# Kernel optimization log

Measured on AMD Instinct MI355X. Metric: run time of the kernel, lower is better.

## Reference

```python
import jax, jax.numpy as jnp
import numpy as np

GRID_RES = (8, 8, 4)      # probe grid -> 256 probes
GRID_MIN = 0.0
GRID_MAX = 1.0
RES = 128                  # cubemap face resolution (max_res)
N_QUERY = 524288


def _cube_face_uv(d):
    """Map unit directions [N,3] -> (face id [N], u [N], v [N]) with the standard
    OpenGL/nvdiffrast cubemap convention (boundary_mode='cube')."""
    x, y, z = d[:, 0], d[:, 1], d[:, 2]
    ax, ay, az = jnp.abs(x), jnp.abs(y), jnp.abs(z)
    is_x = (ax >= ay) & (ax >= az)
    is_y = (~is_x) & (ay >= az)
    face = jnp.where(is_x, jnp.where(x >= 0, 0, 1),
           jnp.where(is_y, jnp.where(y >= 0, 2, 3),
                           jnp.where(z >= 0, 4, 5))).astype(jnp.int32)
    ma = jnp.maximum(jnp.where(is_x, ax, jnp.where(is_y, ay, az)), 1e-9)
    sc = jnp.where(is_x, jnp.where(x >= 0, -z, z),
         jnp.where(is_y, x, jnp.where(z >= 0, x, -x)))
    tc = jnp.where(is_x, -y, jnp.where(is_y, jnp.where(y >= 0, z, -z), -y))
    u = 0.5 * (sc / ma + 1.0)
    v = 0.5 * (tc / ma + 1.0)
    return face, u, v


def _trilinear_corners(xyz):
    """Faithful port of MultiEnvLight._compute_trilinear_corners.
    xyz: [N,3] -> (corner probe indices [N,8] int32, normalized weights [N,8])."""
    res_f = jnp.array(GRID_RES, dtype=jnp.float32)
    res_i = jnp.array(GRID_RES, dtype=jnp.int32)
    span = jnp.maximum(GRID_MAX - GRID_MIN, 1e-6)
    coord = (xyz - GRID_MIN) / span * (res_f - 1.0)
    coord = jnp.clip(coord, 0.0, res_f - 1.0)
    i0 = jnp.floor(coord).astype(jnp.int32)
    i1 = jnp.minimum(i0 + 1, res_i - 1)
    t = coord - i0.astype(jnp.float32)
    # 8 corner offsets (ox, oy, oz)
    offs = jnp.array([[ox, oy, oz] for ox in (0, 1) for oy in (0, 1) for oz in (0, 1)],
                     dtype=jnp.int32)                                  # [8,3]
    idx = jnp.where(offs[None] == 1, i1[:, None, :], i0[:, None, :])   # [N,8,3]
    w = jnp.prod(jnp.where(offs[None] == 1, t[:, None, :], 1.0 - t[:, None, :]), axis=-1)  # [N,8]
    stride_x = GRID_RES[1] * GRID_RES[2]
    stride_y = GRID_RES[2]
    flat = idx[..., 0] * stride_x + idx[..., 1] * stride_y + idx[..., 2]  # [N,8]
    w = w / jnp.maximum(jnp.sum(w, axis=1, keepdims=True), 1e-8)
    return flat, w


def setup_inputs() -> dict:
    key = jax.random.key(0)
    k1, k2, k3 = jax.random.split(key, 3)
    xyz = jax.random.uniform(k1, (N_QUERY, 3), dtype=jnp.float32)
    l = jax.random.normal(k2, (N_QUERY, 3), dtype=jnp.float32)
    n_probes = GRID_RES[0] * GRID_RES[1] * GRID_RES[2]
    base = jax.random.normal(k3, (n_probes, 6, RES, RES, 3), dtype=jnp.float32)
    return {"xyz": xyz, "l": l, "base": base}


def reference(xyz, l, base):
    """MultiEnvLight forward, 'pure_env' mode: trilinear k-NN probe selection over
    the grid + bilinear cube-texture sampling of each selected probe's cubemap,
    weighted blend, then sigmoid()*10 (EnvLight output transform)."""
    R = RES
    d = l / jnp.maximum(jnp.linalg.norm(l, axis=-1, keepdims=True), 1e-9)
    face, u, v = _cube_face_uv(d)
    # bilinear texel footprint (clamp-to-edge within the face)
    fx = u * R - 0.5
    fy = v * R - 0.5
    x0f = jnp.floor(fx)
    y0f = jnp.floor(fy)
    tx = fx - x0f
    ty = fy - y0f
    x0 = jnp.clip(x0f.astype(jnp.int32), 0, R - 1)
    x1 = jnp.clip(x0f.astype(jnp.int32) + 1, 0, R - 1)
    y0 = jnp.clip(y0f.astype(jnp.int32), 0, R - 1)
    y1 = jnp.clip(y0f.astype(jnp.int32) + 1, 0, R - 1)

    pidx, pw = _trilinear_corners(xyz)                       # [N,8], [N,8]
    probe_off = pidx * (6 * R * R) + face[:, None] * (R * R)  # [N,8]
    tap = jnp.stack([y0 * R + x0, y0 * R + x1, y1 * R + x0, y1 * R + x1], axis=-1)  # [N,4]
    taps = probe_off[:, :, None] + tap[:, None, :]            # [N,8,4]
    tapw = jnp.stack([(1.0 - ty) * (1.0 - tx), (1.0 - ty) * tx,
                      ty * (1.0 - tx), ty * tx], axis=-1)     # [N,4]

    vals = base.reshape(-1, 3)[taps]                          # [N,8,4,3] gather
    bil = jnp.einsum('nt,nptc->npc', tapw, vals)              # bilinear per probe
    light = jnp.einsum('np,npc->nc', pw, bil)                 # blend 8 corner probes
    return jax.nn.sigmoid(light) * 10.0
```

## Files before the change

kernel.cpp:

```cpp
#include <hip/hip_runtime.h>
#include <math.h>

#define RES 128

__global__ __launch_bounds__(256) void mel_kernel(
    const float* __restrict__ xyz, const float* __restrict__ l,
    const float* __restrict__ base, float* __restrict__ out, int n)
{
    int i = blockIdx.x * blockDim.x + threadIdx.x;
    if (i >= n) return;

    float lx = l[3*i+0], ly = l[3*i+1], lz = l[3*i+2];
    float nrm = sqrtf(lx*lx + ly*ly + lz*lz);
    float inv = 1.0f / fmaxf(nrm, 1e-9f);
    float dx = lx*inv, dy = ly*inv, dz = lz*inv;

    float ax = fabsf(dx), ay = fabsf(dy), az = fabsf(dz);
    bool is_x = (ax >= ay) && (ax >= az);
    bool is_y = (!is_x) && (ay >= az);

    int face;
    float ma, sc, tc;
    if (is_x) {
        face = (dx >= 0.0f) ? 0 : 1;
        ma = ax;
        sc = (dx >= 0.0f) ? -dz : dz;
        tc = -dy;
    } else if (is_y) {
        face = (dy >= 0.0f) ? 2 : 3;
        ma = ay;
        sc = dx;
        tc = (dy >= 0.0f) ? dz : -dz;
    } else {
        face = (dz >= 0.0f) ? 4 : 5;
        ma = az;
        sc = (dz >= 0.0f) ? dx : -dx;
        tc = -dy;
    }
    ma = fmaxf(ma, 1e-9f);
    float u = 0.5f * (sc / ma + 1.0f);
    float v = 0.5f * (tc / ma + 1.0f);

    float fx = u * (float)RES - 0.5f;
    float fy = v * (float)RES - 0.5f;
    float x0f = floorf(fx), y0f = floorf(fy);
    float tx = fx - x0f, ty = fy - y0f;
    int x0 = min(max((int)x0f,     0), RES-1);
    int x1 = min(max((int)x0f + 1, 0), RES-1);
    int y0 = min(max((int)y0f,     0), RES-1);
    int y1 = min(max((int)y0f + 1, 0), RES-1);

    float px = xyz[3*i+0], py = xyz[3*i+1], pz = xyz[3*i+2];
    float cx = fminf(fmaxf(px * 7.0f, 0.0f), 7.0f);
    float cy = fminf(fmaxf(py * 7.0f, 0.0f), 7.0f);
    float cz = fminf(fmaxf(pz * 3.0f, 0.0f), 3.0f);
    int ix0 = (int)floorf(cx), iy0 = (int)floorf(cy), iz0 = (int)floorf(cz);
    int ix1 = min(ix0 + 1, 7), iy1 = min(iy0 + 1, 7), iz1 = min(iz0 + 1, 3);
    float tgx = cx - (float)ix0, tgy = cy - (float)iy0, tgz = cz - (float)iz0;

    float wx[2] = {1.0f - tgx, tgx};
    float wy[2] = {1.0f - tgy, tgy};
    float wz[2] = {1.0f - tgz, tgz};
    int   gx[2] = {ix0, ix1}, gy[2] = {iy0, iy1}, gz[2] = {iz0, iz1};

    float pw[8];
    int   pidx[8];
    float wsum = 0.0f;
    #pragma unroll
    for (int ox = 0; ox < 2; ++ox)
      #pragma unroll
      for (int oy = 0; oy < 2; ++oy)
        #pragma unroll
        for (int oz = 0; oz < 2; ++oz) {
            int p = ox*4 + oy*2 + oz;
            float w = wx[ox] * wy[oy] * wz[oz];
            pw[p]   = w;
            wsum   += w;
            pidx[p] = gx[ox]*32 + gy[oy]*4 + gz[oz];
        }
    float winv = 1.0f / fmaxf(wsum, 1e-8f);

    int t00 = y0*RES + x0;
    int t01 = y0*RES + x1;
    int t10 = y1*RES + x0;
    int t11 = y1*RES + x1;
    float bw[4];
    bw[0] = (1.0f - ty) * (1.0f - tx);
    bw[1] = (1.0f - ty) * tx;
    bw[2] = ty * (1.0f - tx);
    bw[3] = ty * tx;

    int face_off = face * (RES * RES);
    int toff[4] = {t00, t01, t10, t11};

    float vals[8][4][3];
    #pragma unroll
    for (int p = 0; p < 8; ++p) {
        const float* bp = base + (size_t)(pidx[p] * (6 * RES * RES) + face_off) * 3;
        #pragma unroll
        for (int t = 0; t < 4; ++t) {
            const float* a = bp + toff[t] * 3;
            vals[p][t][0] = a[0];
            vals[p][t][1] = a[1];
            vals[p][t][2] = a[2];
        }
    }

    __builtin_amdgcn_sched_barrier(0);

    float acc0 = 0.0f, acc1 = 0.0f, acc2 = 0.0f;
    #pragma unroll
    for (int p = 0; p < 8; ++p) {
        float w = pw[p];
        #pragma unroll
        for (int t = 0; t < 4; ++t) {
            float wt = w * bw[t];
            acc0 += wt * vals[p][t][0];
            acc1 += wt * vals[p][t][1];
            acc2 += wt * vals[p][t][2];
        }
    }
    acc0 *= winv; acc1 *= winv; acc2 *= winv;

    float s0 = 10.0f / (1.0f + __expf(-acc0));
    float s1 = 10.0f / (1.0f + __expf(-acc1));
    float s2 = 10.0f / (1.0f + __expf(-acc2));

    out[3*i+0] = s0;
    out[3*i+1] = s1;
    out[3*i+2] = s2;
}

extern "C" void kernel_launch(void* const* d_in, const int* in_sizes, int n_in,
                              void* d_out, int out_size, void* d_ws, size_t ws_size,
                              hipStream_t stream) {
    const float* xyz  = (const float*)d_in[0];
    const float* l    = (const float*)d_in[1];
    const float* base = (const float*)d_in[2];
    float* out = (float*)d_out;
    int n = in_sizes[0] / 3;
    int blocks = (n + 255) / 256;
    mel_kernel<<<blocks, 256, 0, stream>>>(xyz, l, base, out, n);
}
```

Baseline: 500.4 us.

## Split each query across four lanes, one per xy probe pair, shuffle-reduce

Each query is now handled by four threads, each gathering the two probes (z corners) for one xy corner, instead of one thread gathering all eight probes. Partial sums and weight sums are combined with xor shuffles, and lane 0 applies the normalization and sigmoid. This cuts per-thread register pressure and serial gather latency to raise occupancy and memory-level parallelism. In exchange, the cubemap direction and grid math is repeated in all four lanes, and three of every four lanes sit idle during the store.

```diff
diff --git a/kernel.cpp b/kernel.cpp
--- a/kernel.cpp
+++ b/kernel.cpp
@@ -7,10 +7,12 @@
     const float* __restrict__ xyz, const float* __restrict__ l,
     const float* __restrict__ base, float* __restrict__ out, int n)
 {
-    int i = blockIdx.x * blockDim.x + threadIdx.x;
-    if (i >= n) return;
+    int tid = blockIdx.x * blockDim.x + threadIdx.x;
+    int q   = tid >> 2;
+    int sub = tid & 3;
+    if (q >= n) return;
 
-    float lx = l[3*i+0], ly = l[3*i+1], lz = l[3*i+2];
+    float lx = l[3*q+0], ly = l[3*q+1], lz = l[3*q+2];
     float nrm = sqrtf(lx*lx + ly*ly + lz*lz);
     float inv = 1.0f / fmaxf(nrm, 1e-9f);
     float dx = lx*inv, dy = ly*inv, dz = lz*inv;
@@ -50,7 +52,7 @@
     int y0 = min(max((int)y0f,     0), RES-1);
     int y1 = min(max((int)y0f + 1, 0), RES-1);
 
-    float px = xyz[3*i+0], py = xyz[3*i+1], pz = xyz[3*i+2];
+    float px = xyz[3*q+0], py = xyz[3*q+1], pz = xyz[3*q+2];
     float cx = fminf(fmaxf(px * 7.0f, 0.0f), 7.0f);
     float cy = fminf(fmaxf(py * 7.0f, 0.0f), 7.0f);
     float cz = fminf(fmaxf(pz * 3.0f, 0.0f), 3.0f);
@@ -58,32 +60,19 @@
     int ix1 = min(ix0 + 1, 7), iy1 = min(iy0 + 1, 7), iz1 = min(iz0 + 1, 3);
     float tgx = cx - (float)ix0, tgy = cy - (float)iy0, tgz = cz - (float)iz0;
 
-    float wx[2] = {1.0f - tgx, tgx};
-    float wy[2] = {1.0f - tgy, tgy};
-    float wz[2] = {1.0f - tgz, tgz};
-    int   gx[2] = {ix0, ix1}, gy[2] = {iy0, iy1}, gz[2] = {iz0, iz1};
+    int   ox  = sub >> 1, oy = sub & 1;
+    float wxf = ox ? tgx : (1.0f - tgx);
+    float wyf = oy ? tgy : (1.0f - tgy);
+    int   gxi = ox ? ix1 : ix0;
+    int   gyi = oy ? iy1 : iy0;
+    float wxy = wxf * wyf;
+    float pw0 = wxy * (1.0f - tgz);
+    float pw1 = wxy * tgz;
+    int   gb  = gxi*32 + gyi*4;
+    int   p0  = gb + iz0;
+    int   p1  = gb + iz1;
 
-    float pw[8];
-    int   pidx[8];
-    float wsum = 0.0f;
-    #pragma unroll
-    for (int ox = 0; ox < 2; ++ox)
-      #pragma unroll
-      for (int oy = 0; oy < 2; ++oy)
-        #pragma unroll
-        for (int oz = 0; oz < 2; ++oz) {
-            int p = ox*4 + oy*2 + oz;
-            float w = wx[ox] * wy[oy] * wz[oz];
-            pw[p]   = w;
-            wsum   += w;
-            pidx[p] = gx[ox]*32 + gy[oy]*4 + gz[oz];
-        }
-    float winv = 1.0f / fmaxf(wsum, 1e-8f);
-
-    int t00 = y0*RES + x0;
-    int t01 = y0*RES + x1;
-    int t10 = y1*RES + x0;
-    int t11 = y1*RES + x1;
+    int toff[4] = { y0*RES + x0, y0*RES + x1, y1*RES + x0, y1*RES + x1 };
     float bw[4];
     bw[0] = (1.0f - ty) * (1.0f - tx);
     bw[1] = (1.0f - ty) * tx;
@@ -91,44 +80,46 @@
     bw[3] = ty * tx;
 
     int face_off = face * (RES * RES);
-    int toff[4] = {t00, t01, t10, t11};
+    const float* bp0 = base + (size_t)(p0 * (6 * RES * RES) + face_off) * 3;
+    const float* bp1 = base + (size_t)(p1 * (6 * RES * RES) + face_off) * 3;
 
-    float vals[8][4][3];
+    float v0[4][3], v1[4][3];
     #pragma unroll
-    for (int p = 0; p < 8; ++p) {
-        const float* bp = base + (size_t)(pidx[p] * (6 * RES * RES) + face_off) * 3;
-        #pragma unroll
-        for (int t = 0; t < 4; ++t) {
-            const float* a = bp + toff[t] * 3;
-            vals[p][t][0] = a[0];
-            vals[p][t][1] = a[1];
-            vals[p][t][2] = a[2];
-        }
+    for (int t = 0; t < 4; ++t) {
+        const float* a = bp0 + toff[t] * 3;
+        v0[t][0] = a[0]; v0[t][1] = a[1]; v0[t][2] = a[2];
+    }
+    #pragma unroll
+    for (int t = 0; t < 4; ++t) {
+        const float* a = bp1 + toff[t] * 3;
+        v1[t][0] = a[0]; v1[t][1] = a[1]; v1[t][2] = a[2];
     }
 
     __builtin_amdgcn_sched_barrier(0);
 
-    float acc0 = 0.0f, acc1 = 0.0f, acc2 = 0.0f;
+    float a0 = 0.0f, a1 = 0.0f, a2 = 0.0f;
     #pragma unroll
-    for (int p = 0; p < 8; ++p) {
-        float w = pw[p];
-        #pragma unroll
-        for (int t = 0; t < 4; ++t) {
-            float wt = w * bw[t];
-            acc0 += wt * vals[p][t][0];
-            acc1 += wt * vals[p][t][1];
-            acc2 += wt * vals[p][t][2];
-        }
+    for (int t = 0; t < 4; ++t) {
+        float w0 = pw0 * bw[t];
+        float w1 = pw1 * bw[t];
+        a0 += w0 * v0[t][0] + w1 * v1[t][0];
+        a1 += w0 * v0[t][1] + w1 * v1[t][1];
+        a2 += w0 * v0[t][2] + w1 * v1[t][2];
     }
-    acc0 *= winv; acc1 *= winv; acc2 *= winv;
+    float ws = pw0 + pw1;
 
-    float s0 = 10.0f / (1.0f + __expf(-acc0));
-    float s1 = 10.0f / (1.0f + __expf(-acc1));
-    float s2 = 10.0f / (1.0f + __expf(-acc2));
+    a0 += __shfl_xor(a0, 1); a1 += __shfl_xor(a1, 1);
+    a2 += __shfl_xor(a2, 1); ws += __shfl_xor(ws, 1);
+    a0 += __shfl_xor(a0, 2); a1 += __shfl_xor(a1, 2);
+    a2 += __shfl_xor(a2, 2); ws += __shfl_xor(ws, 2);
 
-    out[3*i+0] = s0;
-    out[3*i+1] = s1;
-    out[3*i+2] = s2;
+    if (sub == 0) {
+        float winv = 1.0f / fmaxf(ws, 1e-8f);
+        a0 *= winv; a1 *= winv; a2 *= winv;
+        out[3*q+0] = 10.0f / (1.0f + __expf(-a0));
+        out[3*q+1] = 10.0f / (1.0f + __expf(-a1));
+        out[3*q+2] = 10.0f / (1.0f + __expf(-a2));
+    }
 }
 
 extern "C" void kernel_launch(void* const* d_in, const int* in_sizes, int n_in,
@@ -139,6 +130,6 @@
     const float* base = (const float*)d_in[2];
     float* out = (float*)d_out;
     int n = in_sizes[0] / 3;
-    int blocks = (n + 255) / 256;
+    int blocks = (n + 63) / 64;
     mel_kernel<<<blocks, 256, 0, stream>>>(xyz, l, base, out, n);
 }
```

Result: no change. 502.3 us (+0.4%).
